# Kernel tuning notes

Hardware: AMD Instinct MI355X
Metric: run time of the kernel (lower is better)

Reference implementation:

```python
import jax, jax.numpy as jnp
import numpy as np

D = 128        # d_model
VOCAB = 2000   # vocab_size
NUM_ITERS = 6
NUM_V = 98304  # total vertices = 3 * num_edges
NUM_E = NUM_V // 3


def setup_inputs() -> dict:
    key = jax.random.key(0)
    ks = jax.random.split(key, 20)
    std = 0.02
    inp = {
        "x_v": jax.random.randint(ks[0], (NUM_V,), 0, VOCAB),
        "target_mask": jax.random.randint(ks[1], (NUM_V,), 0, 2) > 0,
        # embedding table (vocab_size + 1 rows, last is padding idx)
        "emb": jax.random.normal(ks[2], (VOCAB + 1, D), jnp.float32) * std,
        # edge_init: Linear(1, d_model)
        "edge_init_w": jax.random.normal(ks[3], (D, 1), jnp.float32) * std,
        "edge_init_b": jnp.zeros((D,), jnp.float32),
        # vertex_to_edge LSTM(3d -> d): torch gate order i,f,g,o
        "Wih_v2e": jax.random.normal(ks[4], (4 * D, 3 * D), jnp.float32) * (1.0 / np.sqrt(D)),
        "Whh_v2e": jax.random.normal(ks[5], (4 * D, D), jnp.float32) * (1.0 / np.sqrt(D)),
        "bih_v2e": jax.random.normal(ks[6], (4 * D,), jnp.float32) * (1.0 / np.sqrt(D)),
        "bhh_v2e": jax.random.normal(ks[7], (4 * D,), jnp.float32) * (1.0 / np.sqrt(D)),
        # edge_to_vertex: 3 position-specific LSTM(d -> d), stacked along axis 0
        "Wih_e2v": jax.random.normal(ks[8], (3, 4 * D, D), jnp.float32) * (1.0 / np.sqrt(D)),
        "Whh_e2v": jax.random.normal(ks[9], (3, 4 * D, D), jnp.float32) * (1.0 / np.sqrt(D)),
        "bih_e2v": jax.random.normal(ks[10], (3, 4 * D), jnp.float32) * (1.0 / np.sqrt(D)),
        "bhh_e2v": jax.random.normal(ks[11], (3, 4 * D), jnp.float32) * (1.0 / np.sqrt(D)),
        # output projection Linear(d -> vocab)
        "out_w": jax.random.normal(ks[12], (VOCAB, D), jnp.float32) * std,
        "out_b": jnp.zeros((VOCAB,), jnp.float32),
    }
    return inp


def _lstm_cell(gates, c):
    # torch LSTM gate order: input, forget, cell(g), output
    i, f, g, o = jnp.split(gates, 4, axis=-1)
    c_new = jax.nn.sigmoid(f) * c + jax.nn.sigmoid(i) * jnp.tanh(g)
    h_new = jax.nn.sigmoid(o) * jnp.tanh(c_new)
    return h_new, c_new


def reference(x_v, target_mask, emb, edge_init_w, edge_init_b,
              Wih_v2e, Whh_v2e, bih_v2e, bhh_v2e,
              Wih_e2v, Whh_e2v, bih_e2v, bhh_e2v,
              out_w, out_b):
    E = x_v.shape[0] // 3
    # init embeddings (-1 ids would map to padding row VOCAB; ids are in-range here)
    h_v = emb[x_v].reshape(E, 3, D)              # [E, 3, D]
    c_v = jnp.zeros_like(h_v)
    h_e = jnp.broadcast_to(edge_init_w[:, 0] + edge_init_b, (E, D))  # Linear(1->D) on ones
    c_e = jnp.zeros_like(h_e)
    mask = target_mask.reshape(E, 3)[..., None]  # [E, 3, 1]
    b_v2e = bih_v2e + bhh_v2e                    # [4D]
    b_e2v = (bih_e2v + bhh_e2v)[None]            # [1, 3, 4D]

    for _ in range(NUM_ITERS):
        # vertex -> edge: concat 3 vertices, one LSTM cell step
        msg = h_v.reshape(E, 3 * D)
        gates_e = msg @ Wih_v2e.T + h_e @ Whh_v2e.T + b_v2e          # [E, 4D]
        h_e, c_e = _lstm_cell(gates_e, c_e)
        # edge -> vertex: 3 position-specific LSTM cells, same edge input
        gates_v = (jnp.einsum('ed,pkd->epk', h_e, Wih_e2v)
                   + jnp.einsum('epd,pkd->epk', h_v, Whh_e2v)
                   + b_e2v)                                          # [E, 3, 4D]
        h_new, c_new = _lstm_cell(gates_v, c_v)
        h_v = jnp.where(mask, h_new, h_v)
        c_v = jnp.where(mask, c_new, c_v)

    logits = h_v.reshape(3 * E, D) @ out_w.T + out_b                 # [3E, VOCAB]
    return logits
```

## Files before the change

### kernel.cpp

```cpp
#include <hip/hip_runtime.h>

#define E_CNT 32768
#define V_CNT 98304
#define D_ 128
#define VOCAB_ 2000
#define ITERS_ 6

typedef unsigned short u16;
typedef _Float16 f16;
typedef __attribute__((ext_vector_type(8))) _Float16 f16x8;
typedef __attribute__((ext_vector_type(4))) float f32x4;

__device__ __forceinline__ f32x4 MFh(f16x8 a, f16x8 b, f32x4 c) {
    return __builtin_amdgcn_mfma_f32_16x16x32_f16(a, b, c, 0, 0, 0);
}
__device__ __forceinline__ float sigmoid_f(float x) {
    return __builtin_amdgcn_rcpf(1.0f + __expf(-x));
}
__device__ __forceinline__ float tanh_f(float x) {
    return fmaf(2.0f, __builtin_amdgcn_rcpf(1.0f + __expf(-2.0f * x)), -1.0f);
}

__global__ void detect_mask_kernel(const unsigned int* __restrict__ m, int* __restrict__ flag) {
    int i = blockIdx.x * 256 + threadIdx.x;
    if (i < 4096 && m[i] > 1u) atomicOr(flag, 1);
}

__global__ void prep_kernel(
    const float* __restrict__ Wih_v2e, const float* __restrict__ Whh_v2e,
    const float* __restrict__ bih_v2e, const float* __restrict__ bhh_v2e,
    const float* __restrict__ Wih_e2v, const float* __restrict__ Whh_e2v,
    const float* __restrict__ bih_e2v, const float* __restrict__ bhh_e2v,
    const float* __restrict__ out_w,
    f16* __restrict__ WvF, f16* __restrict__ WeF, f16* __restrict__ OwF,
    float* __restrict__ bv, float* __restrict__ be)
{
    int idx = blockIdx.x * 256 + threadIdx.x;
    if (idx < 262144) {
        const int r = idx & 7, l = (idx >> 3) & 63, t = idx >> 9;
        const int kk = t & 15, nt = t >> 4;
        const int j = nt * 16 + (l & 15);
        const int k = kk * 32 + (l >> 4) * 8 + r;
        const float w = (k < 384) ? Wih_v2e[j * 384 + k] : Whh_v2e[j * 128 + (k - 384)];
        WvF[idx] = (f16)w;
        return;
    }
    idx -= 262144;
    if (idx < 393216) {
        const int r = idx & 7, l = (idx >> 3) & 63, t = idx >> 9;
        const int kk = t & 7, nt = (t >> 3) & 31, p = t >> 8;
        const int j = nt * 16 + (l & 15);
        const int k = kk * 32 + (l >> 4) * 8 + r;
        const float w = (k < 128) ? Wih_e2v[(p * 512 + j) * 128 + k]
                                  : Whh_e2v[(p * 512 + j) * 128 + (k - 128)];
        WeF[idx] = (f16)w;
        return;
    }
    idx -= 393216;
    if (idx < 256000) {
        const int r = idx & 7, l = (idx >> 3) & 63, t = idx >> 9;
        const int kk = t & 3, nt = t >> 2;
        const int j = nt * 16 + (l & 15);
        const int k = kk * 32 + (l >> 4) * 8 + r;
        OwF[idx] = (f16)out_w[j * 128 + k];
        return;
    }
    idx -= 256000;
    if (idx < 512) { bv[idx] = bih_v2e[idx] + bhh_v2e[idx]; return; }
    idx -= 512;
    if (idx < 1536) { be[idx] = bih_e2v[idx] + bhh_e2v[idx]; return; }
}

__global__ __launch_bounds__(512)
void fused_kernel(
    const int* __restrict__ x_v,
    const float* __restrict__ emb,
    const float* __restrict__ eiw, const float* __restrict__ eib,
    const f16* __restrict__ WvF, const f16* __restrict__ WeF,
    const float* __restrict__ bv, const float* __restrict__ be,
    const void* __restrict__ mask, const int* __restrict__ flagp,
    float4* __restrict__ cvG4,
    f16* __restrict__ hvOut)
{
    __shared__ f16 HV[12288];
    __shared__ f16 HE[4096];
    __shared__ char PADL[8704];

    const int tid = threadIdx.x;
    const int c = tid >> 6, l = tid & 63;
    const int lr = l & 15, lk = l >> 4;
    const int e0 = blockIdx.x * 32;

    PADL[tid] = (char)tid;

    for (int i = tid; i < 32 * 48; i += 512) {
        const int row = i / 48, seg = i % 48;
        int id = x_v[(e0 + row) * 3 + (seg >> 4)];
        if (id < 0 || id > VOCAB_) id = VOCAB_;
        const float* s = emb + id * D_ + ((seg * 8) & 127);
        float4 a = *(const float4*)s, b = *(const float4*)(s + 4);
        f16x8 H;
        H[0] = (f16)a.x; H[1] = (f16)a.y; H[2] = (f16)a.z; H[3] = (f16)a.w;
        H[4] = (f16)b.x; H[5] = (f16)b.y; H[6] = (f16)b.z; H[7] = (f16)b.w;
        *(f16x8*)&HV[((row >> 4) * 12 + (seg >> 2)) * 512 + (seg & 3) * 128 + (row & 15) * 8] = H;
    }
    if (tid < 512) {
        const int i = tid;
        const int row = i / 16, seg = i % 16;
        f16x8 H;
        #pragma unroll
        for (int j = 0; j < 8; ++j) H[j] = (f16)(eiw[seg * 8 + j] + eib[seg * 8 + j]);
        *(f16x8*)&HE[((row >> 4) * 4 + (seg >> 2)) * 512 + (seg & 3) * 128 + (row & 15) * 8] = H;
    }

    const int isByte = *flagp;
    unsigned mbits0 = 0, mbits1 = 0, mbits2 = 0;
    #pragma unroll
    for (int p = 0; p < 3; ++p) {
        unsigned mb = 0;
        #pragma unroll
        for (int mt = 0; mt < 2; ++mt)
            #pragma unroll
            for (int r = 0; r < 4; ++r) {
                const int v = (e0 + mt * 16 + lk * 4 + r) * 3 + p;
                const bool m = isByte ? (((const unsigned char*)mask)[v] != 0)
                                      : (((const int*)mask)[v] != 0);
                mb |= (unsigned)m << (mt * 4 + r);
            }
        if (p == 0) mbits0 = mb; else if (p == 1) mbits1 = mb; else mbits2 = mb;
    }
    const int d = c * 16 + lr;
    const int wBase = (c >> 1) * 512 + ((c & 1) * 2 + (lr >> 3)) * 128 + lk * 32 + (lr & 7);
    f32x4 ce[2];
    ce[0] = (f32x4)0.0f; ce[1] = (f32x4)0.0f;

    __syncthreads();
    {
        int keep = (int)PADL[(tid + 1) & 511];
        asm volatile("" :: "v"(keep));
    }

    const f16* HVl = HV + l * 8;
    const f16* HEl = HE + l * 8;
    const size_t cvBase = (size_t)blockIdx.x * 6 * 512 + tid;

    #pragma unroll 1
    for (int it = 0; it < ITERS_; ++it) {
        #pragma unroll 1
        for (int ph = 0; ph < 4; ++ph) {
            const int  nkk = (ph == 0) ? 16 : 8;
            const int  ksp = (ph == 0) ? 12 : 4;
            const f16* pa  = (ph == 0) ? HVl : HEl;
            const int  sa  = (ph == 0) ? 12 : 4;
            const f16* pb  = (ph == 0) ? HEl : HVl;
            const int  sb  = (ph == 0) ? 4 : 12;
            const int  ob  = (ph == 0) ? 0 : (ph - 1) * 4;
            const f16* Wp  = (ph == 0) ? WvF : (WeF + (size_t)(ph - 1) * 131072);
            const float* bp = (ph == 0) ? bv : (be + (ph - 1) * 512);
            const unsigned mb = (ph == 0) ? 0xFFu
                              : ((ph == 1) ? mbits0 : ((ph == 2) ? mbits1 : mbits2));
            f16* wdst = (ph == 0) ? HE : HV;
            const int wstr = (ph == 0) ? 2048 : 6144;
            const int woff = (ph == 0) ? 0 : (ph - 1) * 2048;

            f32x4 acc[2][4];
            #pragma unroll
            for (int g = 0; g < 4; ++g) {
                const float bg = bp[g * 128 + d];
                acc[0][g] = (f32x4)bg;
                acc[1][g] = (f32x4)bg;
            }
            #pragma unroll 1
            for (int kk = 0; kk < nkk; ++kk) {
                const bool lo = kk < ksp;
                f16x8 Ah[2];
                #pragma unroll
                for (int mt = 0; mt < 2; ++mt) {
                    const f16* src = lo ? pa : pb;
                    const int fi = lo ? (mt * sa + kk) : (mt * sb + ob + (kk - ksp));
                    Ah[mt] = *(const f16x8*)(src + fi * 512);
                }
                #pragma unroll
                for (int g = 0; g < 4; ++g) {
                    f16x8 B = *(const f16x8*)(Wp + (size_t)((g * 8 + c) * nkk + kk) * 512 + l * 8);
                    acc[0][g] = MFh(Ah[0], B, acc[0][g]);
                    acc[1][g] = MFh(Ah[1], B, acc[1][g]);
                }
            }
            __syncthreads();

            #pragma unroll
            for (int mt = 0; mt < 2; ++mt) {
                const size_t ci = cvBase + (size_t)((ph - 1) * 2 + mt) * 512;
                float cvv[4];
                if (ph == 0) {
                    #pragma unroll
                    for (int r = 0; r < 4; ++r) cvv[r] = ce[mt][r];
                } else if (it > 0) {
                    float4 t = cvG4[ci];
                    cvv[0] = t.x; cvv[1] = t.y; cvv[2] = t.z; cvv[3] = t.w;
                } else {
                    cvv[0] = cvv[1] = cvv[2] = cvv[3] = 0.0f;
                }
                #pragma unroll
                for (int r = 0; r < 4; ++r) {
                    if ((mb >> (mt * 4 + r)) & 1u) {
                        float gi = sigmoid_f(acc[mt][0][r]);
                        float gf = sigmoid_f(acc[mt][1][r]);
                        float gg = tanh_f(acc[mt][2][r]);
                        float go = sigmoid_f(acc[mt][3][r]);
                        float cn = gf * cvv[r] + gi * gg;
                        cvv[r] = cn;
                        wdst[wBase + mt * wstr + woff + r * 8] = (f16)(go * tanh_f(cn));
                    }
                }
                if (ph == 0) {
                    #pragma unroll
                    for (int r = 0; r < 4; ++r) ce[mt][r] = cvv[r];
                } else {
                    cvG4[ci] = make_float4(cvv[0], cvv[1], cvv[2], cvv[3]);
                }
            }
            if (ph == 0 || ph == 3) __syncthreads();
        }
    }

    for (int i = tid; i < 32 * 48; i += 512) {
        const int row = i / 48, seg = i % 48;
        *(f16x8*)&hvOut[(size_t)(e0 + row) * 384 + seg * 8] =
            *(const f16x8*)&HV[((row >> 4) * 12 + (seg >> 2)) * 512 + (seg & 3) * 128 + (row & 15) * 8];
    }
}

__global__ __launch_bounds__(256) void proj_kernel(
    const f16* __restrict__ hv, const f16* __restrict__ WF,
    const float* __restrict__ out_b, float* __restrict__ out)
{
    __shared__ char occ_pad[49152];
    const int tid = threadIdx.x, l = tid & 63;
    occ_pad[tid] = (char)tid;
    __syncthreads();
    {
        int keep = (int)occ_pad[(tid + 1) & 255];
        asm volatile("" :: "v"(keep));
    }

    const int wid = blockIdx.x * 4 + (tid >> 6);
    const int v0 = wid * 32;
    const int lr = l & 15, lk = l >> 4;

    f16x8 Bv[2][4];
    #pragma unroll
    for (int vt = 0; vt < 2; ++vt)
        #pragma unroll
        for (int kk = 0; kk < 4; ++kk)
            Bv[vt][kk] = *(const f16x8*)(hv + (v0 + vt * 16 + lr) * D_ + kk * 32 + lk * 8);

    f16x8 Wc[4];
    #pragma unroll
    for (int kk = 0; kk < 4; ++kk)
        Wc[kk] = *(const f16x8*)(WF + (kk * 64 + l) * 8);

    #pragma unroll 2
    for (int nt = 0; nt < 125; ++nt) {
        f16x8 Wn[4];
        if (nt < 124) {
            #pragma unroll
            for (int kk = 0; kk < 4; ++kk)
                Wn[kk] = *(const f16x8*)(WF + (((nt + 1) * 4 + kk) * 64 + l) * 8);
        }
        f32x4 a0 = (f32x4)0.0f, a1 = (f32x4)0.0f;
        #pragma unroll
        for (int kk = 0; kk < 4; ++kk) {
            a0 = MFh(Wc[kk], Bv[0][kk], a0);
            a1 = MFh(Wc[kk], Bv[1][kk], a1);
        }
        const int n0 = nt * 16 + lk * 4;
        const float4 bb = *(const float4*)&out_b[n0];
        {
            const size_t v = (size_t)(v0 + lr);
            float4 o = make_float4(a0[0] + bb.x, a0[1] + bb.y, a0[2] + bb.z, a0[3] + bb.w);
            *(float4*)&out[v * VOCAB_ + n0] = o;
        }
        {
            const size_t v = (size_t)(v0 + 16 + lr);
            float4 o = make_float4(a1[0] + bb.x, a1[1] + bb.y, a1[2] + bb.z, a1[3] + bb.w);
            *(float4*)&out[v * VOCAB_ + n0] = o;
        }
        #pragma unroll
        for (int q = 0; q < 4; ++q) Wc[q] = Wn[q];
    }
}

extern "C" void kernel_launch(void* const* d_in, const int* in_sizes, int n_in,
                              void* d_out, int out_size, void* d_ws, size_t ws_size,
                              hipStream_t stream)
{
    const int*   x_v     = (const int*)  d_in[0];
    const void*  mask    = d_in[1];
    const float* emb     = (const float*)d_in[2];
    const float* eiw     = (const float*)d_in[3];
    const float* eib     = (const float*)d_in[4];
    const float* Wih_v2e = (const float*)d_in[5];
    const float* Whh_v2e = (const float*)d_in[6];
    const float* bih_v2e = (const float*)d_in[7];
    const float* bhh_v2e = (const float*)d_in[8];
    const float* Wih_e2v = (const float*)d_in[9];
    const float* Whh_e2v = (const float*)d_in[10];
    const float* bih_e2v = (const float*)d_in[11];
    const float* bhh_e2v = (const float*)d_in[12];
    const float* out_w   = (const float*)d_in[13];
    const float* out_b   = (const float*)d_in[14];
    float* out = (float*)d_out;

    char* ws = (char*)d_ws;
    f16*    hv   = (f16*)(ws);
    f16*    WvF  = (f16*)(ws + 25165824);
    f16*    WeF  = (f16*)(ws + 25690112);
    f16*    OwF  = (f16*)(ws + 26476544);
    float*  bv   = (float*)(ws + 26988544);
    float*  be   = (float*)(ws + 26990592);
    int*    flag = (int*)(ws + 26996736);
    float4* cvG4 = (float4*)(ws + 27000832);

    hipMemsetAsync(flag, 0, 4, stream);
    detect_mask_kernel<<<16, 256, 0, stream>>>((const unsigned int*)mask, flag);
    prep_kernel<<<3568, 256, 0, stream>>>(Wih_v2e, Whh_v2e, bih_v2e, bhh_v2e,
                                          Wih_e2v, Whh_e2v, bih_e2v, bhh_e2v, out_w,
                                          WvF, WeF, OwF, bv, be);
    fused_kernel<<<E_CNT / 32, 512, 0, stream>>>(x_v, emb, eiw, eib,
                                                 WvF, WeF, bv, be,
                                                 mask, flag, cvG4, hv);
    proj_kernel<<<V_CNT / 128, 256, 0, stream>>>(hv, OwF, out_b, out);
}
```

Baseline: 735.6 us.

## Keep vertex cell state in registers and fully unroll LSTM phases

Vertex cell states move from a global float4 scratch buffer into per-thread registers. The four-phase runtime loop becomes one explicit v2e block and three macro-expanded e2v phases with fully unrolled k-loops. E2V hidden outputs are buffered in registers and written to shared memory after one barrier, which removes the per-phase barriers. LDS padding grows, apparently to cap occupancy against the extra register pressure, which risks spills or lower occupancy.

```diff
diff --git a/kernel.cpp b/kernel.cpp
--- a/kernel.cpp
+++ b/kernel.cpp
@@ -7,6 +7,7 @@
 #define ITERS_ 6
 
 typedef unsigned short u16;
+typedef unsigned int u32;
 typedef _Float16 f16;
 typedef __attribute__((ext_vector_type(8))) _Float16 f16x8;
 typedef __attribute__((ext_vector_type(4))) float f32x4;
@@ -19,6 +20,12 @@
 }
 __device__ __forceinline__ float tanh_f(float x) {
     return fmaf(2.0f, __builtin_amdgcn_rcpf(1.0f + __expf(-2.0f * x)), -1.0f);
+}
+__device__ __forceinline__ u16 f16bits(f16 h) {
+    union { f16 f; u16 u; } cv; cv.f = h; return cv.u;
+}
+__device__ __forceinline__ f16 bits2f16(u16 u) {
+    union { f16 f; u16 u; } cv; cv.u = u; return cv.f;
 }
 
 __global__ void detect_mask_kernel(const unsigned int* __restrict__ m, int* __restrict__ flag) {
@@ -79,12 +86,11 @@
     const f16* __restrict__ WvF, const f16* __restrict__ WeF,
     const float* __restrict__ bv, const float* __restrict__ be,
     const void* __restrict__ mask, const int* __restrict__ flagp,
-    float4* __restrict__ cvG4,
     f16* __restrict__ hvOut)
 {
     __shared__ f16 HV[12288];
     __shared__ f16 HE[4096];
-    __shared__ char PADL[8704];
+    __shared__ char PADL[24576];
 
     const int tid = threadIdx.x;
     const int c = tid >> 6, l = tid & 63;
@@ -104,9 +110,8 @@
         H[4] = (f16)b.x; H[5] = (f16)b.y; H[6] = (f16)b.z; H[7] = (f16)b.w;
         *(f16x8*)&HV[((row >> 4) * 12 + (seg >> 2)) * 512 + (seg & 3) * 128 + (row & 15) * 8] = H;
     }
-    if (tid < 512) {
-        const int i = tid;
-        const int row = i / 16, seg = i % 16;
+    {
+        const int row = tid / 16, seg = tid % 16;
         f16x8 H;
         #pragma unroll
         for (int j = 0; j < 8; ++j) H[j] = (f16)(eiw[seg * 8 + j] + eib[seg * 8 + j]);
@@ -131,8 +136,11 @@
     }
     const int d = c * 16 + lr;
     const int wBase = (c >> 1) * 512 + ((c & 1) * 2 + (lr >> 3)) * 128 + lk * 32 + (lr & 7);
-    f32x4 ce[2];
-    ce[0] = (f32x4)0.0f; ce[1] = (f32x4)0.0f;
+
+    f32x4 ce0 = (f32x4)0.0f, ce1 = (f32x4)0.0f;
+    f32x4 cv0a = (f32x4)0.0f, cv0b = (f32x4)0.0f;
+    f32x4 cv1a = (f32x4)0.0f, cv1b = (f32x4)0.0f;
+    f32x4 cv2a = (f32x4)0.0f, cv2b = (f32x4)0.0f;
 
     __syncthreads();
     {
@@ -142,87 +150,121 @@
 
     const f16* HVl = HV + l * 8;
     const f16* HEl = HE + l * 8;
-    const size_t cvBase = (size_t)blockIdx.x * 6 * 512 + tid;
+    const f16* WvB = WvF + (size_t)c * 16 * 512 + l * 8;
+    const f16* WeB = WeF + (size_t)c * 8 * 512 + l * 8;
 
     #pragma unroll 1
     for (int it = 0; it < ITERS_; ++it) {
-        #pragma unroll 1
-        for (int ph = 0; ph < 4; ++ph) {
-            const int  nkk = (ph == 0) ? 16 : 8;
-            const int  ksp = (ph == 0) ? 12 : 4;
-            const f16* pa  = (ph == 0) ? HVl : HEl;
-            const int  sa  = (ph == 0) ? 12 : 4;
-            const f16* pb  = (ph == 0) ? HEl : HVl;
-            const int  sb  = (ph == 0) ? 4 : 12;
-            const int  ob  = (ph == 0) ? 0 : (ph - 1) * 4;
-            const f16* Wp  = (ph == 0) ? WvF : (WeF + (size_t)(ph - 1) * 131072);
-            const float* bp = (ph == 0) ? bv : (be + (ph - 1) * 512);
-            const unsigned mb = (ph == 0) ? 0xFFu
-                              : ((ph == 1) ? mbits0 : ((ph == 2) ? mbits1 : mbits2));
-            f16* wdst = (ph == 0) ? HE : HV;
-            const int wstr = (ph == 0) ? 2048 : 6144;
-            const int woff = (ph == 0) ? 0 : (ph - 1) * 2048;
-
+        {
             f32x4 acc[2][4];
             #pragma unroll
             for (int g = 0; g < 4; ++g) {
-                const float bg = bp[g * 128 + d];
-                acc[0][g] = (f32x4)bg;
-                acc[1][g] = (f32x4)bg;
+                const float bg = bv[g * 128 + d];
+                acc[0][g] = (f32x4)bg; acc[1][g] = (f32x4)bg;
             }
-            #pragma unroll 1
-            for (int kk = 0; kk < nkk; ++kk) {
-                const bool lo = kk < ksp;
-                f16x8 Ah[2];
-                #pragma unroll
-                for (int mt = 0; mt < 2; ++mt) {
-                    const f16* src = lo ? pa : pb;
-                    const int fi = lo ? (mt * sa + kk) : (mt * sb + ob + (kk - ksp));
-                    Ah[mt] = *(const f16x8*)(src + fi * 512);
+            #pragma unroll
+            for (int kk = 0; kk < 16; ++kk) {
+                f16x8 A0, A1;
+                if (kk < 12) {
+                    A0 = *(const f16x8*)(HVl + kk * 512);
+                    A1 = *(const f16x8*)(HVl + (12 + kk) * 512);
+                } else {
+                    A0 = *(const f16x8*)(HEl + (kk - 12) * 512);
+                    A1 = *(const f16x8*)(HEl + (4 + kk - 12) * 512);
                 }
                 #pragma unroll
                 for (int g = 0; g < 4; ++g) {
-                    f16x8 B = *(const f16x8*)(Wp + (size_t)((g * 8 + c) * nkk + kk) * 512 + l * 8);
-                    acc[0][g] = MFh(Ah[0], B, acc[0][g]);
-                    acc[1][g] = MFh(Ah[1], B, acc[1][g]);
+                    f16x8 B = *(const f16x8*)(WvB + (size_t)g * 65536 + kk * 512);
+                    acc[0][g] = MFh(A0, B, acc[0][g]);
+                    acc[1][g] = MFh(A1, B, acc[1][g]);
                 }
             }
             __syncthreads();
-
             #pragma unroll
             for (int mt = 0; mt < 2; ++mt) {
-                const size_t ci = cvBase + (size_t)((ph - 1) * 2 + mt) * 512;
-                float cvv[4];
-                if (ph == 0) {
-                    #pragma unroll
-                    for (int r = 0; r < 4; ++r) cvv[r] = ce[mt][r];
-                } else if (it > 0) {
-                    float4 t = cvG4[ci];
-                    cvv[0] = t.x; cvv[1] = t.y; cvv[2] = t.z; cvv[3] = t.w;
-                } else {
-                    cvv[0] = cvv[1] = cvv[2] = cvv[3] = 0.0f;
-                }
+                f32x4& ce = mt ? ce1 : ce0;
                 #pragma unroll
                 for (int r = 0; r < 4; ++r) {
-                    if ((mb >> (mt * 4 + r)) & 1u) {
-                        float gi = sigmoid_f(acc[mt][0][r]);
-                        float gf = sigmoid_f(acc[mt][1][r]);
-                        float gg = tanh_f(acc[mt][2][r]);
-                        float go = sigmoid_f(acc[mt][3][r]);
-                        float cn = gf * cvv[r] + gi * gg;
-                        cvv[r] = cn;
-                        wdst[wBase + mt * wstr + woff + r * 8] = (f16)(go * tanh_f(cn));
-                    }
-                }
-                if (ph == 0) {
-                    #pragma unroll
-                    for (int r = 0; r < 4; ++r) ce[mt][r] = cvv[r];
-                } else {
-                    cvG4[ci] = make_float4(cvv[0], cvv[1], cvv[2], cvv[3]);
+                    float gi = sigmoid_f(acc[mt][0][r]);
+                    float gf = sigmoid_f(acc[mt][1][r]);
+                    float gg = tanh_f(acc[mt][2][r]);
+                    float go = sigmoid_f(acc[mt][3][r]);
+                    float cn = gf * ce[r] + gi * gg;
+                    ce[r] = cn;
+                    HE[wBase + mt * 2048 + r * 8] = (f16)(go * tanh_f(cn));
                 }
             }
-            if (ph == 0 || ph == 3) __syncthreads();
-        }
+            __syncthreads();
+        }
+
+        u32 hh[3][4];
+
+#define E2V_PHASE(P, MB, CVA, CVB)                                              \
+        {                                                                       \
+            f32x4 acc[2][4];                                                    \
+            _Pragma("unroll")                                                   \
+            for (int g = 0; g < 4; ++g) {                                       \
+                const float bg = be[(P) * 512 + g * 128 + d];                   \
+                acc[0][g] = (f32x4)bg; acc[1][g] = (f32x4)bg;                   \
+            }                                                                   \
+            _Pragma("unroll")                                                   \
+            for (int kk = 0; kk < 8; ++kk) {                                    \
+                f16x8 A0, A1;                                                   \
+                if (kk < 4) {                                                   \
+                    A0 = *(const f16x8*)(HEl + kk * 512);                       \
+                    A1 = *(const f16x8*)(HEl + (4 + kk) * 512);                 \
+                } else {                                                        \
+                    A0 = *(const f16x8*)(HVl + ((P) * 4 + kk - 4) * 512);       \
+                    A1 = *(const f16x8*)(HVl + (12 + (P) * 4 + kk - 4) * 512);  \
+                }                                                               \
+                _Pragma("unroll")                                               \
+                for (int g = 0; g < 4; ++g) {                                   \
+                    f16x8 B = *(const f16x8*)(WeB + (size_t)(P) * 131072        \
+                                              + (size_t)g * 32768 + kk * 512);  \
+                    acc[0][g] = MFh(A0, B, acc[0][g]);                          \
+                    acc[1][g] = MFh(A1, B, acc[1][g]);                          \
+                }                                                               \
+            }                                                                   \
+            _Pragma("unroll")                                                   \
+            for (int mt = 0; mt < 2; ++mt) {                                    \
+                f32x4& cv = mt ? (CVB) : (CVA);                                 \
+                u16 hb[4];                                                      \
+                _Pragma("unroll")                                               \
+                for (int r = 0; r < 4; ++r) {                                   \
+                    float gi = sigmoid_f(acc[mt][0][r]);                        \
+                    float gf = sigmoid_f(acc[mt][1][r]);                        \
+                    float gg = tanh_f(acc[mt][2][r]);                           \
+                    float go = sigmoid_f(acc[mt][3][r]);                        \
+                    float cn = gf * cv[r] + gi * gg;                            \
+                    if (((MB) >> (mt * 4 + r)) & 1u) cv[r] = cn;                \
+                    hb[r] = f16bits((f16)(go * tanh_f(cn)));                    \
+                }                                                               \
+                hh[P][mt * 2]     = (u32)hb[0] | ((u32)hb[1] << 16);            \
+                hh[P][mt * 2 + 1] = (u32)hb[2] | ((u32)hb[3] << 16);            \
+            }                                                                   \
+        }
+
+        E2V_PHASE(0, mbits0, cv0a, cv0b)
+        E2V_PHASE(1, mbits1, cv1a, cv1b)
+        E2V_PHASE(2, mbits2, cv2a, cv2b)
+#undef E2V_PHASE
+
+        __syncthreads();
+
+        #pragma unroll
+        for (int p = 0; p < 3; ++p) {
+            const unsigned mb = (p == 0) ? mbits0 : ((p == 1) ? mbits1 : mbits2);
+            #pragma unroll
+            for (int mt = 0; mt < 2; ++mt)
+                #pragma unroll
+                for (int r = 0; r < 4; ++r)
+                    if ((mb >> (mt * 4 + r)) & 1u) {
+                        u32 w = hh[p][mt * 2 + (r >> 1)];
+                        u16 hb = (r & 1) ? (u16)(w >> 16) : (u16)(w & 0xFFFF);
+                        HV[wBase + mt * 6144 + p * 2048 + r * 8] = bits2f16(hb);
+                    }
+        }
+        __syncthreads();
     }
 
     for (int i = tid; i < 32 * 48; i += 512) {
@@ -321,7 +363,6 @@
     float*  bv   = (float*)(ws + 26988544);
     float*  be   = (float*)(ws + 26990592);
     int*    flag = (int*)(ws + 26996736);
-    float4* cvG4 = (float4*)(ws + 27000832);
 
     hipMemsetAsync(flag, 0, 4, stream);
     detect_mask_kernel<<<16, 256, 0, stream>>>((const unsigned int*)mask, flag);
@@ -330,6 +371,6 @@
                                           WvF, WeF, OwF, bv, be);
     fused_kernel<<<E_CNT / 32, 512, 0, stream>>>(x_v, emb, eiw, eib,
                                                  WvF, WeF, bv, be,
-                                                 mask, flag, cvG4, hv);
+                                                 mask, flag, hv);
     proj_kernel<<<V_CNT / 128, 256, 0, stream>>>(hv, OwF, out_b, out);
 }
```

Result: slower. 2.662 ms (+261.9%).
